# Optimization experiments

Measured on AMD Instinct MI355X. Metric: run time of the kernel, lower is better.

## Reference

```python
import jax, jax.numpy as jnp
import numpy as np

N = 50000          # graph nodes
M = 800000         # graph edges (avg degree 16)
D = 64             # node_dim == edge_dim
NB_NODES = 3       # NAS cell intermediate states
LEAKY = 0.2
EPS = 1e-5
# (dst_state, src_state, op) -- genotype['topology']
TOPOLOGY = [(1, 0, 'gcn'), (2, 0, 'gcn'), (2, 1, 'identity'), (3, 1, 'gcn'), (3, 2, 'identity')]


def setup_inputs() -> dict:
    key = jax.random.key(0)
    ks = jax.random.split(key, 8)
    w = lambda k, shape: jax.random.normal(k, shape, jnp.float32) * 0.05
    return {
        'V': jax.random.normal(ks[0], (N, D), jnp.float32),
        'E': jax.random.normal(ks[1], (M, D), jnp.float32),
        'src_idx': jax.random.randint(ks[2], (M,), 0, N, jnp.int32),
        'dst_idx': jax.random.randint(ks[3], (M,), 0, N, jnp.int32),
        'W_ops': w(ks[4], (len(TOPOLOGY), D, D)),
        'b_ops': jnp.zeros((len(TOPOLOGY), D), jnp.float32),
        'W_cat': w(ks[5], (NB_NODES * D, D)),
        'b_cat': jnp.zeros((D,), jnp.float32),
        'W_S': w(ks[6], (2 * D + D, D)),
        'b_S': jnp.zeros((D,), jnp.float32),
        'gamma_V': jnp.ones((D,), jnp.float32),
        'beta_V': jnp.zeros((D,), jnp.float32),
        'gamma_E': jnp.ones((D,), jnp.float32),
        'beta_E': jnp.zeros((D,), jnp.float32),
    }


def _leaky(x):
    return jnp.where(x >= 0, x, LEAKY * x)


def _bn(x, gamma, beta):  # training-mode BatchNorm1d over rows
    mu = jnp.mean(x, axis=0)
    var = jnp.var(x, axis=0)
    return gamma * (x - mu) * jax.lax.rsqrt(var + EPS) + beta


def reference(V, E, src_idx, dst_idx, W_ops, b_ops, W_cat, b_cat, W_S, b_S,
              gamma_V, beta_V, gamma_E, beta_E):
    # --- DAG of per-edge ops with sum aggregation (load_genotype / forward loop) ---
    states = [V]
    for dst in range(1, NB_NODES + 1):
        agg = None
        for k, (d, src, op) in enumerate(TOPOLOGY):
            if d != dst:
                continue
            h = states[src]
            if op == 'gcn':  # message-pass op: sum neighbor features over graph edges
                h = jax.ops.segment_sum(h[src_idx], dst_idx, num_segments=N)
            h = h @ W_ops[k] + b_ops[k]  # V_Package linear
            agg = h if agg is None else agg + h
        states.append(agg)

    # trans_concat_V over all intermediate states: [N, NB*D] @ [NB*D, D]
    V_new = jnp.concatenate(states[1:], axis=1) @ W_cat + b_cat

    # edge update: S(concat[V_src, leaky(E_in), V_dst])
    E_act = _leaky(E)
    E_new = jnp.concatenate([V_new[src_idx], E_act, V_new[dst_idx]], axis=-1) @ W_S + b_S

    # BN + LeakyReLU + residual (dropout is identity in eval / p=0)
    V_out = _leaky(_bn(V_new, gamma_V, beta_V)) + V
    E_out = _leaky(_bn(E_new, gamma_E, beta_E)) + E
    return (V_out, E_out)
```

## Files before the change

### kernel.cpp

```cpp
#include <hip/hip_runtime.h>
#include <hip/hip_bf16.h>

#define N_NODES 50000
#define M_EDGES 800000
#define LEAKY_F 0.2f
#define BN_EPS 1e-5f
#define NEBLK (M_EDGES / 64)
#define NVBLK ((N_NODES + 63) / 64)
#define NSB ((N_NODES + 255) / 256)

typedef short bf16x8 __attribute__((ext_vector_type(8)));
typedef float f32x4 __attribute__((ext_vector_type(4)));

__device__ __forceinline__ float leaky(float x) { return x >= 0.f ? x : LEAKY_F * x; }

__device__ __forceinline__ unsigned f2bf(float f) {
  unsigned u = __float_as_uint(f);
  return (u + 0x7fffu + ((u >> 16) & 1u)) >> 16;
}
__device__ __forceinline__ unsigned packbf(float a, float b) {
  return (f2bf(b) << 16) | f2bf(a);
}
__device__ __forceinline__ float bflo(unsigned u) { return __uint_as_float(u << 16); }
__device__ __forceinline__ float bfhi(unsigned u) { return __uint_as_float(u & 0xffff0000u); }

__global__ __launch_bounds__(256) void hist_k(const int* __restrict__ dst,
                                              int* __restrict__ counts) {
  int e = blockIdx.x * 256 + threadIdx.x;
  if (e < M_EDGES) atomicAdd(&counts[dst[e]], 1);
}

__global__ __launch_bounds__(256) void blocksum_k(const int* __restrict__ counts,
                                                  int* __restrict__ bsum) {
  __shared__ int wsum[4];
  int tid = threadIdx.x;
  int i = blockIdx.x * 256 + tid;
  int v = (i < N_NODES) ? counts[i] : 0;
#pragma unroll
  for (int off = 32; off; off >>= 1) v += __shfl_down(v, off);
  if ((tid & 63) == 0) wsum[tid >> 6] = v;
  __syncthreads();
  if (tid == 0) bsum[blockIdx.x] = wsum[0] + wsum[1] + wsum[2] + wsum[3];
}

__global__ __launch_bounds__(256) void scanb_k(int* __restrict__ bsum) {
  __shared__ int s[256];
  int tid = threadIdx.x;
  s[tid] = (tid < NSB) ? bsum[tid] : 0;
  __syncthreads();
  for (int off = 1; off < 256; off <<= 1) {
    int v = 0;
    if (tid >= off) v = s[tid - off];
    __syncthreads();
    if (tid >= off) s[tid] += v;
    __syncthreads();
  }
  if (tid < NSB) bsum[tid] = (tid == 0) ? 0 : s[tid - 1];
}

__global__ __launch_bounds__(256) void offs_k(const int* __restrict__ counts,
                                              const int* __restrict__ bsum,
                                              int* __restrict__ offs,
                                              int* __restrict__ cursor) {
  __shared__ int s[256];
  int tid = threadIdx.x;
  int i = blockIdx.x * 256 + tid;
  int c = (i < N_NODES) ? counts[i] : 0;
  s[tid] = c;
  __syncthreads();
  for (int off = 1; off < 256; off <<= 1) {
    int v = 0;
    if (tid >= off) v = s[tid - off];
    __syncthreads();
    if (tid >= off) s[tid] += v;
    __syncthreads();
  }
  int excl = s[tid] - c + bsum[blockIdx.x];
  if (i < N_NODES) {
    offs[i] = excl;
    cursor[i] = excl;
  }
  if (i == N_NODES - 1) offs[N_NODES] = M_EDGES;
}

__global__ __launch_bounds__(256) void fill_k(const int* __restrict__ src,
                                              const int* __restrict__ dst,
                                              int* __restrict__ cursor,
                                              int* __restrict__ ssrc) {
  int e = blockIdx.x * 256 + threadIdx.x;
  if (e >= M_EDGES) return;
  int p = atomicAdd(&cursor[dst[e]], 1);
  ssrc[p] = src[e];
}

__global__ __launch_bounds__(256) void convbf_k(const float* __restrict__ X,
                                                unsigned* __restrict__ Xb, int n4) {
  int i = blockIdx.x * 256 + threadIdx.x;
  if (i >= n4) return;
  const float4* s4 = reinterpret_cast<const float4*>(X) + (size_t)i * 2;
  float4 a = s4[0], b = s4[1];
  uint4 o;
  o.x = packbf(a.x, a.y);
  o.y = packbf(a.z, a.w);
  o.z = packbf(b.x, b.y);
  o.w = packbf(b.z, b.w);
  reinterpret_cast<uint4*>(Xb)[i] = o;
}

__global__ __launch_bounds__(256) void gatherb_k(const unsigned* __restrict__ Xb,
                                                 const int* __restrict__ offs,
                                                 const int* __restrict__ ssrc,
                                                 unsigned* __restrict__ Ob) {
  int n = blockIdx.x * 4 + (threadIdx.x >> 6);
  int lane = threadIdx.x & 63;
  int half = lane >> 5, col = lane & 31;
  int beg = offs[n], end = offs[n + 1];
  float a0 = 0.f, a1 = 0.f;
  int i = beg + half;
  for (; i + 6 < end; i += 8) {
    int s0 = ssrc[i], s1 = ssrc[i + 2], s2 = ssrc[i + 4], s3 = ssrc[i + 6];
    unsigned u0 = Xb[(size_t)s0 * 32 + col];
    unsigned u1 = Xb[(size_t)s1 * 32 + col];
    unsigned u2 = Xb[(size_t)s2 * 32 + col];
    unsigned u3 = Xb[(size_t)s3 * 32 + col];
    a0 += (bflo(u0) + bflo(u1)) + (bflo(u2) + bflo(u3));
    a1 += (bfhi(u0) + bfhi(u1)) + (bfhi(u2) + bfhi(u3));
  }
  for (; i < end; i += 2) {
    unsigned u = Xb[(size_t)ssrc[i] * 32 + col];
    a0 += bflo(u);
    a1 += bfhi(u);
  }
  a0 += __shfl_xor(a0, 32);
  a1 += __shfl_xor(a1, 32);
  if (half == 0) Ob[(size_t)n * 32 + col] = packbf(a0, a1);
}

__global__ __launch_bounds__(256) void prep1_k(const float* __restrict__ W_ops,
                                               const float* __restrict__ W_cat,
                                               float* __restrict__ W12g,
                                               float* __restrict__ Wc12g) {
  __shared__ float Wa[4096], Wb[4096];
  int tid = threadIdx.x;
  const float *Am, *Bm, *Add;
  float* Out;
  if (blockIdx.x == 0) { Am = W_ops; Bm = W_ops + 8192; Add = W_ops + 4096; Out = W12g; }
  else { Am = W_ops + 16384; Bm = W_cat + 8192; Add = W_cat + 4096; Out = Wc12g; }
  for (int i = tid; i < 4096; i += 256) { Wa[i] = Am[i]; Wb[i] = Bm[i]; }
  __syncthreads();
  for (int t = 0; t < 16; ++t) {
    int o = tid + t * 256;
    int r = o >> 6, j = o & 63;
    float acc = Add[o];
#pragma unroll
    for (int k = 0; k < 64; ++k) acc = fmaf(Wa[r * 64 + k], Wb[k * 64 + j], acc);
    Out[o] = acc;
  }
}

__global__ __launch_bounds__(256) void prep2_k(const float* __restrict__ W_ops,
                                               const float* __restrict__ b_ops,
                                               const float* __restrict__ W_cat,
                                               const float* __restrict__ b_cat,
                                               const float* __restrict__ W12g,
                                               const float* __restrict__ Wc12g,
                                               float* __restrict__ WAg,
                                               float* __restrict__ WBg,
                                               float* __restrict__ cg) {
  __shared__ float M0[4096], M1[4096], M2[4096], M3[4096], M4[4096];
  __shared__ float bb[64];
  int tid = threadIdx.x;
  if (blockIdx.x == 0) {
    for (int i = tid; i < 4096; i += 256) {
      M0[i] = W_ops[i];
      M1[i] = W_cat[i];
      M2[i] = W12g[i];
      M3[i] = Wc12g[i];
    }
    __syncthreads();
    for (int t = 0; t < 16; ++t) {
      int o = tid + t * 256;
      int r = o >> 6, j = o & 63;
      float acc = 0.f;
#pragma unroll
      for (int k = 0; k < 64; ++k) {
        acc = fmaf(M0[r * 64 + k], M1[k * 64 + j], acc);
        acc = fmaf(M2[r * 64 + k], M3[k * 64 + j], acc);
      }
      WAg[o] = acc;
    }
  } else {
    for (int i = tid; i < 4096; i += 256) {
      M0[i] = W_ops[3 * 4096 + i];
      M1[i] = W_cat[8192 + i];
      M2[i] = W_ops[2 * 4096 + i];
      M3[i] = W_cat[i];
      M4[i] = Wc12g[i];
    }
    __syncthreads();
    for (int t = 0; t < 16; ++t) {
      int o = tid + t * 256;
      int r = o >> 6, j = o & 63;
      float acc = 0.f;
#pragma unroll
      for (int k = 0; k < 64; ++k) acc = fmaf(M0[r * 64 + k], M1[k * 64 + j], acc);
      WBg[o] = acc;
    }
    if (tid < 64) {
      int j = tid;
      float acc = b_ops[64 + j] + b_ops[128 + j];
#pragma unroll
      for (int k = 0; k < 64; ++k) acc = fmaf(b_ops[k], M2[k * 64 + j], acc);
      bb[j] = acc;
    }
    __syncthreads();
    if (tid < 64) {
      int j = tid;
      float acc = b_cat[j];
#pragma unroll
      for (int k = 0; k < 64; ++k) {
        acc = fmaf(b_ops[k], M3[k * 64 + j], acc);
        acc = fmaf(bb[k], M4[k * 64 + j], acc);
        acc = fmaf(b_ops[192 + k] + b_ops[256 + k], M1[k * 64 + j], acc);
      }
      cg[j] = acc;
    }
  }
}

__global__ __launch_bounds__(256) void prep3_k(const float* __restrict__ W_ops,
                                               const float* __restrict__ b_ops,
                                               const float* __restrict__ WBg,
                                               float* __restrict__ W0Bg,
                                               float* __restrict__ b0Bg) {
  __shared__ float Wa[4096], Wb[4096];
  int tid = threadIdx.x;
  for (int i = tid; i < 4096; i += 256) { Wa[i] = W_ops[i]; Wb[i] = WBg[i]; }
  __syncthreads();
  for (int t = 0; t < 16; ++t) {
    int o = tid + t * 256;
    int r = o >> 6, j = o & 63;
    float acc = 0.f;
#pragma unroll
    for (int k = 0; k < 64; ++k) acc = fmaf(Wa[r * 64 + k], Wb[k * 64 + j], acc);
    W0Bg[o] = acc;
  }
  if (tid < 64) {
    float acc = 0.f;
#pragma unroll
    for (int k = 0; k < 64; ++k) acc = fmaf(b_ops[k], Wb[k * 64 + tid], acc);
    b0Bg[tid] = acc;
  }
}

__global__ __launch_bounds__(256) void prepW_k(
    const float* __restrict__ WAg, const float* __restrict__ W0Bg,
    const float* __restrict__ W_S,
    unsigned* __restrict__ WAF, unsigned* __restrict__ W0BF,
    unsigned* __restrict__ Ws0F, unsigned* __restrict__ Ws2F,
    unsigned* __restrict__ WmF) {
  const float* src;
  unsigned* dst;
  switch (blockIdx.x) {
    case 0: src = WAg; dst = WAF; break;
    case 1: src = W0Bg; dst = W0BF; break;
    case 2: src = W_S; dst = Ws0F; break;
    case 3: src = W_S + 8192; dst = Ws2F; break;
    default: src = W_S + 4096; dst = WmF; break;
  }
  for (int q = threadIdx.x; q < 2048; q += 256) {
    int ui = q & 3, ln = (q >> 2) & 63, t = q >> 8;
    int jt = t >> 1, kh = t & 1;
    int j = jt * 16 + (ln & 15);
    int k2 = kh * 16 + (ln >> 4) * 4 + ui;
    dst[q] = packbf(src[(2 * k2) * 64 + j], src[(2 * k2 + 1) * 64 + j]);
  }
}

__global__ __launch_bounds__(256) void vnewproj_k(
    const unsigned* __restrict__ Ab, const unsigned* __restrict__ Cb,
    const int* __restrict__ counts,
    const unsigned* __restrict__ WAF, const unsigned* __restrict__ W0BF,
    const unsigned* __restrict__ Ws0F, const unsigned* __restrict__ Ws2F,
    const float* __restrict__ cg, const float* __restrict__ b0Bg,
    const float* __restrict__ b_S,
    float* __restrict__ Vnew, unsigned* __restrict__ PsP, unsigned* __restrict__ PdP) {
  __shared__ __align__(16) unsigned AF[2048], CF[2048], VF[2048];
  __shared__ float cb[64], b0v[64], bsv[64];
  int tid = threadIdx.x;
  int n0 = blockIdx.x * 64;
  for (int q = tid; q < 2048; q += 256) {
    int r = q >> 5, k2 = q & 31;
    int row = n0 + r;
    if (row >= N_NODES) row = N_NODES - 1;
    unsigned ua = Ab[(size_t)row * 32 + k2];
    unsigned uc = Cb[(size_t)row * 32 + k2];
    int kh = k2 >> 4, k2h = k2 & 15;
    int ln = (r & 15) + 16 * (k2h >> 2);
    int idx = ((((r >> 4) << 1) + kh) * 64 + ln) * 4 + (k2h & 3);
    AF[idx] = ua;
    CF[idx] = uc;
  }
  if (tid < 64) { cb[tid] = cg[tid]; b0v[tid] = b0Bg[tid]; bsv[tid] = b_S[tid]; }
  __syncthreads();

  int lane = tid & 63, et = tid >> 6;
  int col15 = lane & 15, g4 = lane >> 4;
  float deg[4];
#pragma unroll
  for (int reg = 0; reg < 4; ++reg) {
    int rg = n0 + et * 16 + g4 * 4 + reg;
    deg[reg] = (float)counts[rg < N_NODES ? rg : N_NODES - 1];
  }
  f32x4 a0 = {0.f, 0.f, 0.f, 0.f}, a1 = a0, a2 = a0, a3 = a0;
#pragma unroll
  for (int kh = 0; kh < 2; ++kh) {
    uint4 au = *reinterpret_cast<const uint4*>(&AF[(((et << 1) + kh) * 64 + lane) * 4]);
    uint4 cu = *reinterpret_cast<const uint4*>(&CF[(((et << 1) + kh) * 64 + lane) * 4]);
    bf16x8 afr = *reinterpret_cast<bf16x8*>(&au);
    bf16x8 cfr = *reinterpret_cast<bf16x8*>(&cu);
    uint4 wa0 = *reinterpret_cast<const uint4*>(&WAF[((0 * 2 + kh) * 64 + lane) * 4]);
    uint4 wa1 = *reinterpret_cast<const uint4*>(&WAF[((1 * 2 + kh) * 64 + lane) * 4]);
    uint4 wa2 = *reinterpret_cast<const uint4*>(&WAF[((2 * 2 + kh) * 64 + lane) * 4]);
    uint4 wa3 = *reinterpret_cast<const uint4*>(&WAF[((3 * 2 + kh) * 64 + lane) * 4]);
    uint4 wc0 = *reinterpret_cast<const uint4*>(&W0BF[((0 * 2 + kh) * 64 + lane) * 4]);
    uint4 wc1 = *reinterpret_cast<const uint4*>(&W0BF[((1 * 2 + kh) * 64 + lane) * 4]);
    uint4 wc2 = *reinterpret_cast<const uint4*>(&W0BF[((2 * 2 + kh) * 64 + lane) * 4]);
    uint4 wc3 = *reinterpret_cast<const uint4*>(&W0BF[((3 * 2 + kh) * 64 + lane) * 4]);
    a0 = __builtin_amdgcn_mfma_f32_16x16x32_bf16(afr, *reinterpret_cast<bf16x8*>(&wa0), a0, 0, 0, 0);
    a1 = __builtin_amdgcn_mfma_f32_16x16x32_bf16(afr, *reinterpret_cast<bf16x8*>(&wa1), a1, 0, 0, 0);
    a2 = __builtin_amdgcn_mfma_f32_16x16x32_bf16(afr, *reinterpret_cast<bf16x8*>(&wa2), a2, 0, 0, 0);
    a3 = __builtin_amdgcn_mfma_f32_16x16x32_bf16(afr, *reinterpret_cast<bf16x8*>(&wa3), a3, 0, 0, 0);
    a0 = __builtin_amdgcn_mfma_f32_16x16x32_bf16(cfr, *reinterpret_cast<bf16x8*>(&wc0), a0, 0, 0, 0);
    a1 = __builtin_amdgcn_mfma_f32_16x16x32_bf16(cfr, *reinterpret_cast<bf16x8*>(&wc1), a1, 0, 0, 0);
    a2 = __builtin_amdgcn_mfma_f32_16x16x32_bf16(cfr, *reinterpret_cast<bf16x8*>(&wc2), a2, 0, 0, 0);
    a3 = __builtin_amdgcn_mfma_f32_16x16x32_bf16(cfr, *reinterpret_cast<bf16x8*>(&wc3), a3, 0, 0, 0);
  }
#pragma unroll
  for (int jt = 0; jt < 4; ++jt) {
    f32x4 a = (jt == 0) ? a0 : (jt == 1) ? a1 : (jt == 2) ? a2 : a3;
    int j = jt * 16 + col15;
#pragma unroll
    for (int reg = 0; reg < 4; ++reg) {
      float v = a[reg] + fmaf(deg[reg], b0v[j], cb[j]);
      a[reg] = v;
      int rg = n0 + et * 16 + g4 * 4 + reg;
      if (rg < N_NODES) Vnew[(size_t)rg * 64 + j] = v;
    }
#pragma unroll
    for (int reg = 0; reg < 4; ++reg) {
      float v = a[reg];
      float pv = __shfl_xor(v, 1);
      if (!(col15 & 1)) {
        int k2p = jt * 8 + (col15 >> 1);
        int kh2 = k2p >> 4, k2h = k2p & 15;
        int ln = (g4 * 4 + reg) + 16 * (k2h >> 2);
        VF[(((et << 1) + kh2) * 64 + ln) * 4 + (k2h & 3)] = packbf(v, pv);
      }
    }
  }
  __syncthreads();
  f32x4 p0 = {0.f, 0.f, 0.f, 0.f}, p1 = p0, p2 = p0, p3 = p0;
  f32x4 d0 = p0, d1 = p0, d2 = p0, d3 = p0;
#pragma unroll
  for (int kh = 0; kh < 2; ++kh) {
    uint4 vu = *reinterpret_cast<const uint4*>(&VF[(((et << 1) + kh) * 64 + lane) * 4]);
    bf16x8 vfr = *reinterpret_cast<bf16x8*>(&vu);
    uint4 w00 = *reinterpret_cast<const uint4*>(&Ws0F[((0 * 2 + kh) * 64 + lane) * 4]);
    uint4 w01 = *reinterpret_cast<const uint4*>(&Ws0F[((1 * 2 + kh) * 64 + lane) * 4]);
    uint4 w02 = *reinterpret_cast<const uint4*>(&Ws0F[((2 * 2 + kh) * 64 + lane) * 4]);
    uint4 w03 = *reinterpret_cast<const uint4*>(&Ws0F[((3 * 2 + kh) * 64 + lane) * 4]);
    uint4 w20 = *reinterpret_cast<const uint4*>(&Ws2F[((0 * 2 + kh) * 64 + lane) * 4]);
    uint4 w21 = *reinterpret_cast<const uint4*>(&Ws2F[((1 * 2 + kh) * 64 + lane) * 4]);
    uint4 w22 = *reinterpret_cast<const uint4*>(&Ws2F[((2 * 2 + kh) * 64 + lane) * 4]);
    uint4 w23 = *reinterpret_cast<const uint4*>(&Ws2F[((3 * 2 + kh) * 64 + lane) * 4]);
    p0 = __builtin_amdgcn_mfma_f32_16x16x32_bf16(vfr, *reinterpret_cast<bf16x8*>(&w00), p0, 0, 0, 0);
    p1 = __builtin_amdgcn_mfma_f32_16x16x32_bf16(vfr, *reinterpret_cast<bf16x8*>(&w01), p1, 0, 0, 0);
    p2 = __builtin_amdgcn_mfma_f32_16x16x32_bf16(vfr, *reinterpret_cast<bf16x8*>(&w02), p2, 0, 0, 0);
    p3 = __builtin_amdgcn_mfma_f32_16x16x32_bf16(vfr, *reinterpret_cast<bf16x8*>(&w03), p3, 0, 0, 0);
    d0 = __builtin_amdgcn_mfma_f32_16x16x32_bf16(vfr, *reinterpret_cast<bf16x8*>(&w20), d0, 0, 0, 0);
    d1 = __builtin_amdgcn_mfma_f32_16x16x32_bf16(vfr, *reinterpret_cast<bf16x8*>(&w21), d1, 0, 0, 0);
    d2 = __builtin_amdgcn_mfma_f32_16x16x32_bf16(vfr, *reinterpret_cast<bf16x8*>(&w22), d2, 0, 0, 0);
    d3 = __builtin_amdgcn_mfma_f32_16x16x32_bf16(vfr, *reinterpret_cast<bf16x8*>(&w23), d3, 0, 0, 0);
  }
#pragma unroll
  for (int pt = 0; pt < 4; ++pt) {
    f32x4 p = (pt == 0) ? p0 : (pt == 1) ? p1 : (pt == 2) ? p2 : p3;
    f32x4 d = (pt == 0) ? d0 : (pt == 1) ? d1 : (pt == 2) ? d2 : d3;
    int pj = pt * 16 + col15;
#pragma unroll
    for (int reg = 0; reg < 4; ++reg) {
      float vp = p[reg] + bsv[pj];
      float vd = d[reg];
      float pvp = __shfl_xor(vp, 1);
      float pvd = __shfl_xor(vd, 1);
      if (!(col15 & 1)) {
        int rg = n0 + et * 16 + g4 * 4 + reg;
        if (rg < N_NODES) {
          PsP[(size_t)rg * 32 + pt * 8 + (col15 >> 1)] = packbf(vp, pvp);
          PdP[(size_t)rg * 32 + pt * 8 + (col15 >> 1)] = packbf(vd, pvd);
        }
      }
    }
  }
}

__global__ __launch_bounds__(256) void edge_k(
    const float* __restrict__ Eg, const int* __restrict__ src, const int* __restrict__ dst,
    const unsigned* __restrict__ PsP, const unsigned* __restrict__ PdP,
    const unsigned* __restrict__ WmF, unsigned* __restrict__ EoutSlots,
    float* __restrict__ partials) {
  __shared__ __align__(16) unsigned EaF[2048];
  __shared__ unsigned Spd[64][34];
  __shared__ float ls[128];
  int tid = threadIdx.x;
  int e0 = blockIdx.x * 64;
  int l16 = tid & 15, g16 = tid >> 4;

  uint2 pa[4], pb[4];
#pragma unroll
  for (int rr = 0; rr < 4; ++rr) {
    int p = e0 + rr * 16 + g16;
    int s = src[p], d = dst[p];
    pa[rr] = *reinterpret_cast<const uint2*>(&PsP[(size_t)s * 32 + 2 * l16]);
    pb[rr] = *reinterpret_cast<const uint2*>(&PdP[(size_t)d * 32 + 2 * l16]);
  }
  if (tid < 128) ls[tid] = 0.f;
  for (int q = tid; q < 1024; q += 256) {
    int e = q >> 4, kq = q & 15;
    float4 vv = reinterpret_cast<const float4*>(Eg)[(size_t)(e0 + e) * 16 + kq];
    unsigned u0 = packbf(leaky(vv.x), leaky(vv.y));
    unsigned u1 = packbf(leaky(vv.z), leaky(vv.w));
    int k2a = 2 * kq;
    int kh = k2a >> 4, k2h = k2a & 15;
    int lane = (e & 15) + 16 * (k2h >> 2);
    int base = ((((e >> 4) << 1) + kh) * 64 + lane) * 4 + (k2h & 3);
    EaF[base] = u0;
    EaF[base + 1] = u1;
  }
#pragma unroll
  for (int rr = 0; rr < 4; ++rr) {
    int r = rr * 16 + g16;
    float fx = bflo(pa[rr].x) + bflo(pb[rr].x);
    float fy = bfhi(pa[rr].x) + bfhi(pb[rr].x);
    float fz = bflo(pa[rr].y) + bflo(pb[rr].y);
    float fw = bfhi(pa[rr].y) + bfhi(pb[rr].y);
    *reinterpret_cast<uint2*>(&Spd[r][l16 * 2]) = make_uint2(packbf(fx, fy), packbf(fz, fw));
  }
  __syncthreads();

  int lane = tid & 63;
  int et = tid >> 6;
  f32x4 acc0 = {0.f, 0.f, 0.f, 0.f};
  f32x4 acc1 = acc0, acc2 = acc0, acc3 = acc0;
#pragma unroll
  for (int kh = 0; kh < 2; ++kh) {
    uint4 au = *reinterpret_cast<const uint4*>(&EaF[(((et << 1) + kh) * 64 + lane) * 4]);
    bf16x8 afr = *reinterpret_cast<bf16x8*>(&au);
    uint4 b0 = *reinterpret_cast<const uint4*>(&WmF[((0 * 2 + kh) * 64 + lane) * 4]);
    uint4 b1 = *reinterpret_cast<const uint4*>(&WmF[((1 * 2 + kh) * 64 + lane) * 4]);
    uint4 b2 = *reinterpret_cast<const uint4*>(&WmF[((2 * 2 + kh) * 64 + lane) * 4]);
    uint4 b3 = *reinterpret_cast<const uint4*>(&WmF[((3 * 2 + kh) * 64 + lane) * 4]);
    acc0 = __builtin_amdgcn_mfma_f32_16x16x32_bf16(afr, *reinterpret_cast<bf16x8*>(&b0), acc0, 0, 0, 0);
    acc1 = __builtin_amdgcn_mfma_f32_16x16x32_bf16(afr, *reinterpret_cast<bf16x8*>(&b1), acc1, 0, 0, 0);
    acc2 = __builtin_amdgcn_mfma_f32_16x16x32_bf16(afr, *reinterpret_cast<bf16x8*>(&b2), acc2, 0, 0, 0);
    acc3 = __builtin_amdgcn_mfma_f32_16x16x32_bf16(afr, *reinterpret_cast<bf16x8*>(&b3), acc3, 0, 0, 0);
  }

  int col15 = lane & 15, g4 = lane >> 4;
  float s4[4] = {0.f, 0.f, 0.f, 0.f}, q4[4] = {0.f, 0.f, 0.f, 0.f};
  f32x4 accs[4];
#pragma unroll
  for (int jt = 0; jt < 4; ++jt) {
    f32x4 a = (jt == 0) ? acc0 : (jt == 1) ? acc1 : (jt == 2) ? acc2 : acc3;
#pragma unroll
    for (int reg = 0; reg < 4; ++reg) {
      int e = et * 16 + g4 * 4 + reg;
      int j = jt * 16 + col15;
      unsigned sp = Spd[e][j >> 1];
      float add = (j & 1) ? bfhi(sp) : bflo(sp);
      float v = a[reg] + add;
      a[reg] = v;
      s4[jt] += v;
      q4[jt] = fmaf(v, v, q4[jt]);
    }
    accs[jt] = a;
  }
#pragma unroll
  for (int jt = 0; jt < 4; ++jt) {
#pragma unroll
    for (int reg = 0; reg < 4; ++reg) {
      float v = accs[jt][reg];
      float pv = __shfl_xor(v, 1);
      if (!(col15 & 1)) {
        int e = e0 + et * 16 + g4 * 4 + reg;
        EoutSlots[(size_t)e * 64 + jt * 8 + (col15 >> 1)] = packbf(v, pv);
      }
    }
  }
#pragma unroll
  for (int jt = 0; jt < 4; ++jt) {
    s4[jt] += __shfl_xor(s4[jt], 16);
    q4[jt] += __shfl_xor(q4[jt], 16);
    s4[jt] += __shfl_xor(s4[jt], 32);
    q4[jt] += __shfl_xor(q4[jt], 32);
  }
  if (g4 == 0) {
#pragma unroll
    for (int jt = 0; jt < 4; ++jt) {
      atomicAdd(&ls[jt * 16 + col15], s4[jt]);
      atomicAdd(&ls[64 + jt * 16 + col15], q4[jt]);
    }
  }
  __syncthreads();
  if (tid < 128) partials[(size_t)blockIdx.x * 128 + tid] = ls[tid];
}

__global__ __launch_bounds__(256) void reduce_stats_k(const float* __restrict__ partials,
                                                      float* __restrict__ stats) {
  __shared__ float ls[128];
  int tid = threadIdx.x;
  if (tid < 128) ls[tid] = 0.f;
  __syncthreads();
  int c = tid & 127;
  int half = tid >> 7;
  float s = 0.f;
  for (int r = blockIdx.x * 2 + half; r < NEBLK; r += 2 * gridDim.x) {
    s += partials[(size_t)r * 128 + c];
  }
  atomicAdd(&ls[c], s);
  __syncthreads();
  if (tid < 128) atomicAdd(&stats[tid], ls[tid]);
}

__global__ __launch_bounds__(256) void col_stats_k(
    const float* __restrict__ X, size_t nelem, float* __restrict__ sums) {
  __shared__ float ls[128];
  int tid = threadIdx.x;
  if (tid < 128) ls[tid] = 0.f;
  __syncthreads();
  int j = tid & 63;
  float s = 0.f, ss = 0.f;
  size_t stride = (size_t)gridDim.x * blockDim.x;
  for (size_t i = (size_t)blockIdx.x * blockDim.x + tid; i < nelem; i += stride) {
    float x = X[i];
    s += x;
    ss = fmaf(x, x, ss);
  }
  atomicAdd(&ls[j], s);
  atomicAdd(&ls[64 + j], ss);
  __syncthreads();
  if (tid < 128) atomicAdd(&sums[tid], ls[tid]);
}

__global__ void finalize_k(const float* __restrict__ sums, float inv_n,
                           const float* __restrict__ gamma, const float* __restrict__ beta,
                           float* __restrict__ sc_shift) {
  int j = threadIdx.x;
  float mu = sums[j] * inv_n;
  float var = sums[64 + j] * inv_n - mu * mu;
  float sc = gamma[j] * rsqrtf(var + BN_EPS);
  sc_shift[j] = sc;
  sc_shift[64 + j] = beta[j] - mu * sc;
}

__global__ __launch_bounds__(256) void bn_apply_k(
    float* __restrict__ X, const float* __restrict__ resid,
    const float* __restrict__ sc_shift, int n4) {
  int i = blockIdx.x * blockDim.x + threadIdx.x;
  if (i >= n4) return;
  int jq = i & 15;
  float4 x = reinterpret_cast<float4*>(X)[i];
  float4 r = reinterpret_cast<const float4*>(resid)[i];
  float4 sc = reinterpret_cast<const float4*>(sc_shift)[jq];
  float4 sh = reinterpret_cast<const float4*>(sc_shift + 64)[jq];
  float4 y;
  y.x = leaky(fmaf(x.x, sc.x, sh.x)) + r.x;
  y.y = leaky(fmaf(x.y, sc.y, sh.y)) + r.y;
  y.z = leaky(fmaf(x.z, sc.z, sh.z)) + r.z;
  y.w = leaky(fmaf(x.w, sc.w, sh.w)) + r.w;
  reinterpret_cast<float4*>(X)[i] = y;
}

__global__ __launch_bounds__(256) void bn_applyE_k(
    float* __restrict__ EoutF, const float* __restrict__ Eg,
    const float* __restrict__ sc_shift) {
  __shared__ float scs[128];
  int tid = threadIdx.x;
  if (tid < 128) scs[tid] = sc_shift[tid];
  __syncthreads();
  int i = blockIdx.x * 256 + tid;
  int jq = i & 15;
  float2 pr = reinterpret_cast<const float2*>(EoutF)[((size_t)(i >> 4)) * 32 + jq];
  unsigned u0 = __float_as_uint(pr.x);
  unsigned u1 = __float_as_uint(pr.y);
  float v0 = bflo(u0), v1 = bfhi(u0), v2 = bflo(u1), v3 = bfhi(u1);
  float4 eg = reinterpret_cast<const float4*>(Eg)[i];
  int j = jq * 4;
  float4 o;
  o.x = leaky(fmaf(v0, scs[j + 0], scs[64 + j + 0])) + eg.x;
  o.y = leaky(fmaf(v1, scs[j + 1], scs[64 + j + 1])) + eg.y;
  o.z = leaky(fmaf(v2, scs[j + 2], scs[64 + j + 2])) + eg.z;
  o.w = leaky(fmaf(v3, scs[j + 3], scs[64 + j + 3])) + eg.w;
  reinterpret_cast<float4*>(EoutF)[i] = o;
}

extern "C" void kernel_launch(void* const* d_in, const int* in_sizes, int n_in,
                              void* d_out, int out_size, void* d_ws, size_t ws_size,
                              hipStream_t stream) {
  const float* V      = (const float*)d_in[0];
  const float* Eg     = (const float*)d_in[1];
  const int*   src    = (const int*)d_in[2];
  const int*   dst    = (const int*)d_in[3];
  const float* W_ops  = (const float*)d_in[4];
  const float* b_ops  = (const float*)d_in[5];
  const float* W_cat  = (const float*)d_in[6];
  const float* b_cat  = (const float*)d_in[7];
  const float* W_S    = (const float*)d_in[8];
  const float* b_S    = (const float*)d_in[9];
  const float* gammaV = (const float*)d_in[10];
  const float* betaV  = (const float*)d_in[11];
  const float* gammaE = (const float*)d_in[12];
  const float* betaE  = (const float*)d_in[13];

  float* ws = (float*)d_ws;
  const size_t ND = (size_t)N_NODES * 64;
  const size_t NH = (size_t)N_NODES * 32;
  unsigned* Vb  = (unsigned*)ws;
  unsigned* Ab  = (unsigned*)ws + NH;
  unsigned* Cb  = (unsigned*)ws + 2 * NH;
  unsigned* PsP = (unsigned*)ws + 3 * NH;
  unsigned* PdP = (unsigned*)ws + 4 * NH;
  float* xb   = ws + 5 * NH;
  float* W12g  = xb;
  float* Wc12g = xb + 4096;
  float* WAg   = xb + 8192;
  float* WBg   = xb + 12288;
  float* W0Bg  = xb + 16384;
  float* cg    = xb + 20480;
  float* b0Bg  = xb + 20544;
  float* statsV = xb + 20608;
  float* statsE = statsV + 128;
  float* scshV  = statsV + 256;
  float* scshE  = statsV + 384;
  int* counts = (int*)(statsV + 512);
  int* offs   = counts + N_NODES;
  int* cursor = offs + N_NODES + 1;
  int* ssrc   = cursor + N_NODES;
  float* partials = (float*)(ssrc + M_EDGES);
  unsigned* WAF  = (unsigned*)(partials + (size_t)NEBLK * 128);
  unsigned* W0BF = WAF + 2048;
  unsigned* Ws0F = WAF + 4096;
  unsigned* Ws2F = WAF + 6144;
  unsigned* WmF  = WAF + 8192;
  int* bsum = (int*)(WAF + 10240);

  float* Vout  = (float*)d_out;
  float* EoutF = Vout + ND;
  unsigned* EoutSlots = (unsigned*)EoutF;

  hipMemsetAsync(counts, 0, N_NODES * sizeof(int), stream);
  hipMemsetAsync(statsV, 0, 256 * sizeof(float), stream);

  const int eb = (M_EDGES + 255) / 256;
  prep1_k<<<2, 256, 0, stream>>>(W_ops, W_cat, W12g, Wc12g);
  prep2_k<<<2, 256, 0, stream>>>(W_ops, b_ops, W_cat, b_cat, W12g, Wc12g, WAg, WBg, cg);
  prep3_k<<<1, 256, 0, stream>>>(W_ops, b_ops, WBg, W0Bg, b0Bg);
  prepW_k<<<5, 256, 0, stream>>>(WAg, W0Bg, W_S, WAF, W0BF, Ws0F, Ws2F, WmF);
  hist_k<<<eb, 256, 0, stream>>>(dst, counts);
  blocksum_k<<<NSB, 256, 0, stream>>>(counts, bsum);
  scanb_k<<<1, 256, 0, stream>>>(bsum);
  offs_k<<<NSB, 256, 0, stream>>>(counts, bsum, offs, cursor);
  fill_k<<<eb, 256, 0, stream>>>(src, dst, cursor, ssrc);

  convbf_k<<<(N_NODES * 8 + 255) / 256, 256, 0, stream>>>(V, Vb, N_NODES * 8);
  gatherb_k<<<N_NODES / 4, 256, 0, stream>>>(Vb, offs, ssrc, Ab);
  gatherb_k<<<N_NODES / 4, 256, 0, stream>>>(Ab, offs, ssrc, Cb);
  vnewproj_k<<<NVBLK, 256, 0, stream>>>(Ab, Cb, counts, WAF, W0BF, Ws0F, Ws2F,
                                        cg, b0Bg, b_S, Vout, PsP, PdP);
  edge_k<<<NEBLK, 256, 0, stream>>>(Eg, src, dst, PsP, PdP, WmF, EoutSlots, partials);
  reduce_stats_k<<<64, 256, 0, stream>>>(partials, statsE);
  col_stats_k<<<512, 256, 0, stream>>>(Vout, ND, statsV);
  finalize_k<<<1, 64, 0, stream>>>(statsV, 1.f / N_NODES, gammaV, betaV, scshV);
  finalize_k<<<1, 64, 0, stream>>>(statsE, 1.f / M_EDGES, gammaE, betaE, scshE);
  bn_apply_k<<<(int)((ND / 4 + 255) / 256), 256, 0, stream>>>(Vout, V, scshV, (int)(ND / 4));
  bn_applyE_k<<<M_EDGES * 16 / 256, 256, 0, stream>>>(EoutF, Eg, scshE);
}
```

Before: 474.5 us.

## Fuse second gather and V BN stats into vnewproj, widen gather loads

The second neighbor gather (producing Cb) is folded into vnewproj_k, so each block gathers its own 64 rows' neighbor sums straight into shared memory instead of writing and re-reading a global buffer. vnewproj_k also accumulates per-block column sums and squared sums of Vnew into partials, which replaces the separate col_stats pass over Vout. The two stats reductions and the two finalize kernels are each merged into one launch. The first gatherb_k is rewritten to use 16 lanes per row with 8-byte loads. The trade-off is that the fused gather runs with one 16-lane group per row and less memory-level parallelism per block, which may slow vnewproj.

```diff
diff --git a/kernel.cpp b/kernel.cpp
--- a/kernel.cpp
+++ b/kernel.cpp
@@ -113,27 +113,37 @@
                                                  unsigned* __restrict__ Ob) {
   int n = blockIdx.x * 4 + (threadIdx.x >> 6);
   int lane = threadIdx.x & 63;
-  int half = lane >> 5, col = lane & 31;
+  int grp = lane >> 4, col = lane & 15;
   int beg = offs[n], end = offs[n + 1];
-  float a0 = 0.f, a1 = 0.f;
-  int i = beg + half;
-  for (; i + 6 < end; i += 8) {
-    int s0 = ssrc[i], s1 = ssrc[i + 2], s2 = ssrc[i + 4], s3 = ssrc[i + 6];
-    unsigned u0 = Xb[(size_t)s0 * 32 + col];
-    unsigned u1 = Xb[(size_t)s1 * 32 + col];
-    unsigned u2 = Xb[(size_t)s2 * 32 + col];
-    unsigned u3 = Xb[(size_t)s3 * 32 + col];
-    a0 += (bflo(u0) + bflo(u1)) + (bflo(u2) + bflo(u3));
-    a1 += (bfhi(u0) + bfhi(u1)) + (bfhi(u2) + bfhi(u3));
-  }
-  for (; i < end; i += 2) {
-    unsigned u = Xb[(size_t)ssrc[i] * 32 + col];
-    a0 += bflo(u);
-    a1 += bfhi(u);
-  }
-  a0 += __shfl_xor(a0, 32);
-  a1 += __shfl_xor(a1, 32);
-  if (half == 0) Ob[(size_t)n * 32 + col] = packbf(a0, a1);
+  float a0 = 0.f, a1 = 0.f, a2 = 0.f, a3 = 0.f;
+  int i = beg + grp;
+  for (; i + 4 < end; i += 8) {
+    int s0 = ssrc[i], s1 = ssrc[i + 4];
+    uint2 u0 = *reinterpret_cast<const uint2*>(&Xb[(size_t)s0 * 32 + col * 2]);
+    uint2 u1 = *reinterpret_cast<const uint2*>(&Xb[(size_t)s1 * 32 + col * 2]);
+    a0 += bflo(u0.x) + bflo(u1.x);
+    a1 += bfhi(u0.x) + bfhi(u1.x);
+    a2 += bflo(u0.y) + bflo(u1.y);
+    a3 += bfhi(u0.y) + bfhi(u1.y);
+  }
+  for (; i < end; i += 4) {
+    uint2 u = *reinterpret_cast<const uint2*>(&Xb[(size_t)ssrc[i] * 32 + col * 2]);
+    a0 += bflo(u.x);
+    a1 += bfhi(u.x);
+    a2 += bflo(u.y);
+    a3 += bfhi(u.y);
+  }
+#pragma unroll
+  for (int off = 16; off <= 32; off <<= 1) {
+    a0 += __shfl_xor(a0, off);
+    a1 += __shfl_xor(a1, off);
+    a2 += __shfl_xor(a2, off);
+    a3 += __shfl_xor(a3, off);
+  }
+  if (grp == 0) {
+    uint2 o = make_uint2(packbf(a0, a1), packbf(a2, a3));
+    *reinterpret_cast<uint2*>(&Ob[(size_t)n * 32 + col * 2]) = o;
+  }
 }
 
 __global__ __launch_bounds__(256) void prep1_k(const float* __restrict__ W_ops,
@@ -278,30 +288,65 @@
 }
 
 __global__ __launch_bounds__(256) void vnewproj_k(
-    const unsigned* __restrict__ Ab, const unsigned* __restrict__ Cb,
+    const unsigned* __restrict__ Ab,
+    const int* __restrict__ offs, const int* __restrict__ ssrc,
     const int* __restrict__ counts,
     const unsigned* __restrict__ WAF, const unsigned* __restrict__ W0BF,
     const unsigned* __restrict__ Ws0F, const unsigned* __restrict__ Ws2F,
     const float* __restrict__ cg, const float* __restrict__ b0Bg,
     const float* __restrict__ b_S,
-    float* __restrict__ Vnew, unsigned* __restrict__ PsP, unsigned* __restrict__ PdP) {
+    float* __restrict__ Vnew, unsigned* __restrict__ PsP, unsigned* __restrict__ PdP,
+    float* __restrict__ partialsV) {
   __shared__ __align__(16) unsigned AF[2048], CF[2048], VF[2048];
   __shared__ float cb[64], b0v[64], bsv[64];
+  __shared__ float lsv[128];
   int tid = threadIdx.x;
   int n0 = blockIdx.x * 64;
+  int l16 = tid & 15, g16 = tid >> 4;
+#pragma unroll
+  for (int rr = 0; rr < 4; ++rr) {
+    int r = g16 + 16 * rr;
+    int n = n0 + r;
+    float a0 = 0.f, a1 = 0.f, a2 = 0.f, a3 = 0.f;
+    if (n < N_NODES) {
+      int beg = offs[n], end = offs[n + 1];
+      int i = beg;
+      for (; i + 1 < end; i += 2) {
+        int s0 = ssrc[i], s1 = ssrc[i + 1];
+        uint2 u0 = *reinterpret_cast<const uint2*>(&Ab[(size_t)s0 * 32 + l16 * 2]);
+        uint2 u1 = *reinterpret_cast<const uint2*>(&Ab[(size_t)s1 * 32 + l16 * 2]);
+        a0 += bflo(u0.x) + bflo(u1.x);
+        a1 += bfhi(u0.x) + bfhi(u1.x);
+        a2 += bflo(u0.y) + bflo(u1.y);
+        a3 += bfhi(u0.y) + bfhi(u1.y);
+      }
+      if (i < end) {
+        uint2 u = *reinterpret_cast<const uint2*>(&Ab[(size_t)ssrc[i] * 32 + l16 * 2]);
+        a0 += bflo(u.x);
+        a1 += bfhi(u.x);
+        a2 += bflo(u.y);
+        a3 += bfhi(u.y);
+      }
+    }
+    unsigned pu0 = packbf(a0, a1), pu1 = packbf(a2, a3);
+    int k2 = 2 * l16;
+    int kh = k2 >> 4, k2h = k2 & 15;
+    int ln = (r & 15) + 16 * (k2h >> 2);
+    int base = ((((r >> 4) << 1) + kh) * 64 + ln) * 4 + (k2h & 3);
+    CF[base] = pu0;
+    CF[base + 1] = pu1;
+  }
   for (int q = tid; q < 2048; q += 256) {
     int r = q >> 5, k2 = q & 31;
     int row = n0 + r;
     if (row >= N_NODES) row = N_NODES - 1;
     unsigned ua = Ab[(size_t)row * 32 + k2];
-    unsigned uc = Cb[(size_t)row * 32 + k2];
     int kh = k2 >> 4, k2h = k2 & 15;
     int ln = (r & 15) + 16 * (k2h >> 2);
-    int idx = ((((r >> 4) << 1) + kh) * 64 + ln) * 4 + (k2h & 3);
-    AF[idx] = ua;
-    CF[idx] = uc;
+    AF[((((r >> 4) << 1) + kh) * 64 + ln) * 4 + (k2h & 3)] = ua;
   }
   if (tid < 64) { cb[tid] = cg[tid]; b0v[tid] = b0Bg[tid]; bsv[tid] = b_S[tid]; }
+  if (tid < 128) lsv[tid] = 0.f;
   __syncthreads();
 
   int lane = tid & 63, et = tid >> 6;
@@ -336,6 +381,7 @@
     a2 = __builtin_amdgcn_mfma_f32_16x16x32_bf16(cfr, *reinterpret_cast<bf16x8*>(&wc2), a2, 0, 0, 0);
     a3 = __builtin_amdgcn_mfma_f32_16x16x32_bf16(cfr, *reinterpret_cast<bf16x8*>(&wc3), a3, 0, 0, 0);
   }
+  float s4[4] = {0.f, 0.f, 0.f, 0.f}, q4[4] = {0.f, 0.f, 0.f, 0.f};
 #pragma unroll
   for (int jt = 0; jt < 4; ++jt) {
     f32x4 a = (jt == 0) ? a0 : (jt == 1) ? a1 : (jt == 2) ? a2 : a3;
@@ -345,7 +391,11 @@
       float v = a[reg] + fmaf(deg[reg], b0v[j], cb[j]);
       a[reg] = v;
       int rg = n0 + et * 16 + g4 * 4 + reg;
-      if (rg < N_NODES) Vnew[(size_t)rg * 64 + j] = v;
+      if (rg < N_NODES) {
+        Vnew[(size_t)rg * 64 + j] = v;
+        s4[jt] += v;
+        q4[jt] = fmaf(v, v, q4[jt]);
+      }
     }
 #pragma unroll
     for (int reg = 0; reg < 4; ++reg) {
@@ -359,7 +409,23 @@
       }
     }
   }
-  __syncthreads();
+#pragma unroll
+  for (int jt = 0; jt < 4; ++jt) {
+    s4[jt] += __shfl_xor(s4[jt], 16);
+    q4[jt] += __shfl_xor(q4[jt], 16);
+    s4[jt] += __shfl_xor(s4[jt], 32);
+    q4[jt] += __shfl_xor(q4[jt], 32);
+  }
+  if (g4 == 0) {
+#pragma unroll
+    for (int jt = 0; jt < 4; ++jt) {
+      atomicAdd(&lsv[jt * 16 + col15], s4[jt]);
+      atomicAdd(&lsv[64 + jt * 16 + col15], q4[jt]);
+    }
+  }
+  __syncthreads();
+  if (tid < 128) partialsV[(size_t)blockIdx.x * 128 + tid] = lsv[tid];
+
   f32x4 p0 = {0.f, 0.f, 0.f, 0.f}, p1 = p0, p2 = p0, p3 = p0;
   f32x4 d0 = p0, d1 = p0, d2 = p0, d3 = p0;
 #pragma unroll
@@ -516,52 +582,47 @@
   if (tid < 128) partials[(size_t)blockIdx.x * 128 + tid] = ls[tid];
 }
 
-__global__ __launch_bounds__(256) void reduce_stats_k(const float* __restrict__ partials,
-                                                      float* __restrict__ stats) {
+__global__ __launch_bounds__(256) void reduce2_k(const float* __restrict__ pE,
+                                                 const float* __restrict__ pV,
+                                                 float* __restrict__ statsE,
+                                                 float* __restrict__ statsV) {
   __shared__ float ls[128];
   int tid = threadIdx.x;
   if (tid < 128) ls[tid] = 0.f;
   __syncthreads();
+  bool isV = blockIdx.x >= 64;
+  const float* p = isV ? pV : pE;
+  float* out = isV ? statsV : statsE;
+  int nrows = isV ? NVBLK : NEBLK;
+  int b = isV ? (int)blockIdx.x - 64 : (int)blockIdx.x;
+  int nb = isV ? 8 : 64;
   int c = tid & 127;
   int half = tid >> 7;
   float s = 0.f;
-  for (int r = blockIdx.x * 2 + half; r < NEBLK; r += 2 * gridDim.x) {
-    s += partials[(size_t)r * 128 + c];
+  for (int r = b * 2 + half; r < nrows; r += 2 * nb) {
+    s += p[(size_t)r * 128 + c];
   }
   atomicAdd(&ls[c], s);
   __syncthreads();
-  if (tid < 128) atomicAdd(&stats[tid], ls[tid]);
-}
-
-__global__ __launch_bounds__(256) void col_stats_k(
-    const float* __restrict__ X, size_t nelem, float* __restrict__ sums) {
-  __shared__ float ls[128];
-  int tid = threadIdx.x;
-  if (tid < 128) ls[tid] = 0.f;
-  __syncthreads();
+  if (tid < 128) atomicAdd(&out[tid], ls[tid]);
+}
+
+__global__ void finalize2_k(const float* __restrict__ statsV, const float* __restrict__ statsE,
+                            const float* __restrict__ gammaV, const float* __restrict__ betaV,
+                            const float* __restrict__ gammaE, const float* __restrict__ betaE,
+                            float* __restrict__ scshV, float* __restrict__ scshE) {
+  int tid = threadIdx.x;
   int j = tid & 63;
-  float s = 0.f, ss = 0.f;
-  size_t stride = (size_t)gridDim.x * blockDim.x;
-  for (size_t i = (size_t)blockIdx.x * blockDim.x + tid; i < nelem; i += stride) {
-    float x = X[i];
-    s += x;
-    ss = fmaf(x, x, ss);
-  }
-  atomicAdd(&ls[j], s);
-  atomicAdd(&ls[64 + j], ss);
-  __syncthreads();
-  if (tid < 128) atomicAdd(&sums[tid], ls[tid]);
-}
-
-__global__ void finalize_k(const float* __restrict__ sums, float inv_n,
-                           const float* __restrict__ gamma, const float* __restrict__ beta,
-                           float* __restrict__ sc_shift) {
-  int j = threadIdx.x;
+  const float* sums = (tid < 64) ? statsV : statsE;
+  const float* gamma = (tid < 64) ? gammaV : gammaE;
+  const float* beta = (tid < 64) ? betaV : betaE;
+  float* scsh = (tid < 64) ? scshV : scshE;
+  float inv_n = (tid < 64) ? (1.f / N_NODES) : (1.f / M_EDGES);
   float mu = sums[j] * inv_n;
   float var = sums[64 + j] * inv_n - mu * mu;
   float sc = gamma[j] * rsqrtf(var + BN_EPS);
-  sc_shift[j] = sc;
-  sc_shift[64 + j] = beta[j] - mu * sc;
+  scsh[j] = sc;
+  scsh[64 + j] = beta[j] - mu * sc;
 }
 
 __global__ __launch_bounds__(256) void bn_apply_k(
@@ -628,10 +689,9 @@
   const size_t NH = (size_t)N_NODES * 32;
   unsigned* Vb  = (unsigned*)ws;
   unsigned* Ab  = (unsigned*)ws + NH;
-  unsigned* Cb  = (unsigned*)ws + 2 * NH;
-  unsigned* PsP = (unsigned*)ws + 3 * NH;
-  unsigned* PdP = (unsigned*)ws + 4 * NH;
-  float* xb   = ws + 5 * NH;
+  unsigned* PsP = (unsigned*)ws + 2 * NH;
+  unsigned* PdP = (unsigned*)ws + 3 * NH;
+  float* xb   = ws + 4 * NH;
   float* W12g  = xb;
   float* Wc12g = xb + 4096;
   float* WAg   = xb + 8192;
@@ -648,7 +708,8 @@
   int* cursor = offs + N_NODES + 1;
   int* ssrc   = cursor + N_NODES;
   float* partials = (float*)(ssrc + M_EDGES);
-  unsigned* WAF  = (unsigned*)(partials + (size_t)NEBLK * 128);
+  float* partialsV = partials + (size_t)NEBLK * 128;
+  unsigned* WAF  = (unsigned*)(partialsV + (size_t)NVBLK * 128);
   unsigned* W0BF = WAF + 2048;
   unsigned* Ws0F = WAF + 4096;
   unsigned* Ws2F = WAF + 6144;
@@ -675,14 +736,12 @@
 
   convbf_k<<<(N_NODES * 8 + 255) / 256, 256, 0, stream>>>(V, Vb, N_NODES * 8);
   gatherb_k<<<N_NODES / 4, 256, 0, stream>>>(Vb, offs, ssrc, Ab);
-  gatherb_k<<<N_NODES / 4, 256, 0, stream>>>(Ab, offs, ssrc, Cb);
-  vnewproj_k<<<NVBLK, 256, 0, stream>>>(Ab, Cb, counts, WAF, W0BF, Ws0F, Ws2F,
-                                        cg, b0Bg, b_S, Vout, PsP, PdP);
+  vnewproj_k<<<NVBLK, 256, 0, stream>>>(Ab, offs, ssrc, counts, WAF, W0BF, Ws0F, Ws2F,
+                                        cg, b0Bg, b_S, Vout, PsP, PdP, partialsV);
   edge_k<<<NEBLK, 256, 0, stream>>>(Eg, src, dst, PsP, PdP, WmF, EoutSlots, partials);
-  reduce_stats_k<<<64, 256, 0, stream>>>(partials, statsE);
-  col_stats_k<<<512, 256, 0, stream>>>(Vout, ND, statsV);
-  finalize_k<<<1, 64, 0, stream>>>(statsV, 1.f / N_NODES, gammaV, betaV, scshV);
-  finalize_k<<<1, 64, 0, stream>>>(statsE, 1.f / M_EDGES, gammaE, betaE, scshE);
+  reduce2_k<<<72, 256, 0, stream>>>(partials, partialsV, statsE, statsV);
+  finalize2_k<<<1, 128, 0, stream>>>(statsV, statsE, gammaV, betaV, gammaE, betaE,
+                                     scshV, scshE);
   bn_apply_k<<<(int)((ND / 4 + 255) / 256), 256, 0, stream>>>(Vout, V, scshV, (int)(ND / 4));
   bn_applyE_k<<<M_EDGES * 16 / 256, 256, 0, stream>>>(EoutF, Eg, scshE);
 }
```

After: 457.1 us. 3.7% less time.
